# Performance work log

Measured on AMD Instinct MI355X. Metric: run time of the kernel, lower is better.

The kernel has to match this reference:

```python
import jax, jax.numpy as jnp
import numpy as np

B, N, K, C_IN, D = 4, 2048, 16, 480, 64
EPS = 1e-5


def _c1(x, w, b):
    # 1x1 Conv1d: x (B,C,N), w (O,C) -> (B,O,N)
    return jnp.einsum('oc,bcn->bon', w, x) + b[:, None]


def _c2(x, w, b):
    # 1x1 Conv2d: x (B,C,J,N), w (O,C) -> (B,O,J,N)
    return jnp.einsum('oc,bcjn->bojn', w, x) + b[:, None, None]


def _bn(x, g, b):
    # eval-mode BatchNorm2d with running_mean=0, running_var=1
    return x * (g / jnp.sqrt(1.0 + EPS))[:, None, None] + b[:, None, None]


def _mlp_res(x, w1, b1, w2, b2, ws, bs):
    return _c1(jax.nn.relu(_c1(x, w1, b1)), w2, b2) + _c1(x, ws, bs)


def _group(f, idx):
    # f (B,C,N), idx (B,K,N) int -> out[b,c,j,n] = f[b,c,idx[b,j,n]]  -> (B,C,K,N)
    return jax.vmap(lambda ff, ii: ff[:, ii])(f, idx)


def _knn_idx(xyz):
    # xyz (B,3,N) -> idx (B,K,N), excluding the self point (nearest neighbor)
    pts = xyz.transpose(0, 2, 1)  # (B,N,3)
    sq = jnp.sum(pts * pts, -1)
    d2 = sq[:, :, None] + sq[:, None, :] - 2.0 * jnp.einsum('bnd,bmd->bnm', pts, pts)
    _, idx = jax.lax.top_k(-d2, K + 1)  # (B,N,K+1), nearest first
    return idx.transpose(0, 2, 1)[:, 1:, :]  # drop self -> (B,K,N)


def _forward(idx, feature, xyz, bt1_w, bt1_b, bt2_w, bt2_b, bts_w, bts_b,
             q_w, q_b, k_w, k_b, v_w, v_b,
             fd1_w, fd1_b, fd_g, fd_bb, fd2_w, fd2_b,
             fg1_w, fg1_b, fg_g, fg_bb, fg2_w, fg2_b,
             at_w, at_b, m41_w, m41_b, m42_w, m42_b):
    x = _mlp_res(feature, bt1_w, bt1_b, bt2_w, bt2_b, bts_w, bts_b)  # (B,64,N)
    q = _c1(x, q_w, q_b)
    k = _c1(x, k_w, k_b)
    v = _c1(x, v_w, v_b)

    group_xyz = _group(xyz, idx)                       # (B,3,K,N)
    rel_xyz = xyz[:, :, None, :] - group_xyz           # (B,3,K,N)
    pos_enc = _c2(jax.nn.relu(_bn(_c2(rel_xyz, fd1_w, fd1_b), fd_g, fd_bb)), fd2_w, fd2_b)  # (B,64,K,N)

    k_local = _group(k, idx)                           # (B,64,K,N)
    v_local = _group(v, idx)
    qk_rel = q[:, :, None, :] - k_local
    attn = _c2(jax.nn.relu(_bn(_c2(qk_rel + pos_enc, fg1_w, fg1_b), fg_g, fg_bb)), fg2_w, fg2_b)  # (B,64,K,N)

    attn1 = attn.transpose(0, 1, 3, 2)                 # (B,64,N,K)
    # ConvTranspose2d(64,64,(4,1),(4,1)) with kernel==stride: out[b,o,4n+r,f] = sum_c x[b,c,n,f]*W[c,o,r] + bias[o]
    y = jnp.einsum('bcnf,cor->bonrf', attn1, at_w)
    y = y.reshape(y.shape[0], y.shape[1], -1, y.shape[4]) + at_b[None, :, None, None]  # (B,64,4N,K)
    attn = jax.nn.softmax(y, axis=1)

    value_rel = (v_local + pos_enc).transpose(0, 1, 3, 2)   # (B,64,N,K)
    value = jnp.repeat(value_rel, 4, axis=2)                # nearest upsample (4,1) -> (B,64,4N,K)

    res = jnp.einsum('bmnf,bmnf->bmn', attn, value)         # (B,64,4N)
    identity = jnp.repeat(x, 4, axis=2)                     # nearest upsample x4 -> (B,64,4N)
    res = res + identity
    completion = _c1(jax.nn.relu(_c1(res, m41_w, m41_b)), m42_w, m42_b)  # (B,3,4N)
    return completion, res


def setup_inputs() -> dict:
    key = jax.random.key(0)
    ks = jax.random.split(key, 24)
    i = iter(range(24))

    def w(shape):
        return (jax.random.normal(ks[next(i)], shape, dtype=jnp.float32) * 0.05)

    z = lambda n: jnp.zeros((n,), jnp.float32)
    o = lambda n: jnp.ones((n,), jnp.float32)
    return {
        'feature': jax.random.normal(ks[next(i)], (B, C_IN, N), dtype=jnp.float32),
        'xyz': jax.random.normal(ks[next(i)], (B, 3, N), dtype=jnp.float32),
        'bt1_w': w((D, C_IN)), 'bt1_b': z(D),
        'bt2_w': w((D, D)), 'bt2_b': z(D),
        'bts_w': w((D, C_IN)), 'bts_b': z(D),
        'q_w': w((D, D)), 'q_b': z(D),
        'k_w': w((D, D)), 'k_b': z(D),
        'v_w': w((D, D)), 'v_b': z(D),
        'fd1_w': w((D, 3)), 'fd1_b': z(D), 'fd_g': o(D), 'fd_bb': z(D),
        'fd2_w': w((D, D)), 'fd2_b': z(D),
        'fg1_w': w((4 * D, D)), 'fg1_b': z(4 * D), 'fg_g': o(4 * D), 'fg_bb': z(4 * D),
        'fg2_w': w((D, 4 * D)), 'fg2_b': z(D),
        'at_w': w((D, D, 4)), 'at_b': z(D),
        'm41_w': w((D, D)), 'm41_b': z(D),
        'm42_w': w((3, D)), 'm42_b': z(3),
    }


def reference(feature, xyz, bt1_w, bt1_b, bt2_w, bt2_b, bts_w, bts_b,
              q_w, q_b, k_w, k_b, v_w, v_b,
              fd1_w, fd1_b, fd_g, fd_bb, fd2_w, fd2_b,
              fg1_w, fg1_b, fg_g, fg_bb, fg2_w, fg2_b,
              at_w, at_b, m41_w, m41_b, m42_w, m42_b):
    idx = _knn_idx(xyz)
    return _forward(idx, feature, xyz, bt1_w, bt1_b, bt2_w, bt2_b, bts_w, bts_b,
                    q_w, q_b, k_w, k_b, v_w, v_b,
                    fd1_w, fd1_b, fd_g, fd_bb, fd2_w, fd2_b,
                    fg1_w, fg1_b, fg_g, fg_bb, fg2_w, fg2_b,
                    at_w, at_b, m41_w, m41_b, m42_w, m42_b)
```

## Files before the change

kernel.cpp:

```cpp
#include <hip/hip_runtime.h>

#define B_ 4
#define N_ 2048
#define K_ 16
#define CIN_ 480
#define UPN_ 8192
#define M_ (B_*N_*K_)
#define MX_ (B_*N_)
#define KCAP 448

#define KNN_BLK 2048
#define TR_BLK  1920
#define PREP_BLK 1047

typedef unsigned int u32;
typedef unsigned short u16;
typedef unsigned long long u64;
typedef __attribute__((ext_vector_type(8))) short short8;
typedef __attribute__((ext_vector_type(4))) float f32x4;

#define DEV static __device__ __forceinline__

DEV float b2f(u16 h){ return __uint_as_float(((u32)h)<<16); }
DEV u16 f2b(float f){
  u32 u = __float_as_uint(f);
  u32 r = u + 0x7fffu + ((u>>16)&1u);
  return (u16)(r>>16);
}
DEV u32 cvtpk(float a, float b){
  u32 r; asm("v_cvt_pk_bf16_f32 %0, %1, %2" : "=v"(r) : "v"(a), "v"(b));
  return r;
}
DEV u64 cvtpk4(float a, float b, float c, float d){
  return (u64)cvtpk(a,b) | ((u64)cvtpk(c,d)<<32);
}
DEV bool detect_bf(const void* fg){ return ((((const u32*)fg)[0]) & 0xFFFFu) == 0x3F80u; }
DEV float ld(const void* p, int i, bool bf){
  return bf ? b2f(((const u16*)p)[i]) : ((const float*)p)[i];
}
DEV u64 makekey(float d2, int m){
  u32 bits = __float_as_uint(d2);
  bits = (bits & 0x80000000u) ? ~bits : (bits | 0x80000000u);
  return ((u64)bits<<32) | (u32)m;
}
DEV int swz64 (int row, int colByte){ return row*128 + (colByte ^ ((row&7)<<4)); }
DEV int swz128(int row, int colByte){ return row*256 + (colByte ^ ((row&7)<<4)); }

__global__ __launch_bounds__(256) void setup_kernel(
    const void* __restrict__ feature, const void* __restrict__ xyz,
    const void* __restrict__ bt1_w, const void* __restrict__ bt1_b,
    const void* __restrict__ bt2_w, const void* __restrict__ bt2_b,
    const void* __restrict__ bts_w, const void* __restrict__ bts_b,
    const void* __restrict__ q_w, const void* __restrict__ q_b,
    const void* __restrict__ k_w, const void* __restrict__ k_b,
    const void* __restrict__ v_w, const void* __restrict__ v_b,
    const void* __restrict__ fd1_w, const void* __restrict__ fd1_b,
    const void* __restrict__ fd_g, const void* __restrict__ fd_bb,
    const void* __restrict__ fd2_w, const void* __restrict__ fd2_b,
    const void* __restrict__ fg1_w, const void* __restrict__ fg1_b,
    const void* __restrict__ fg_g, const void* __restrict__ fg_bb,
    const void* __restrict__ fg2_w, const void* __restrict__ fg2_b,
    const void* __restrict__ at_w, const void* __restrict__ at_b,
    const void* __restrict__ m41_w, const void* __restrict__ m41_b,
    const void* __restrict__ m42_w, const void* __restrict__ m42_b,
    float* __restrict__ W, u16* __restrict__ WB,
    u16* __restrict__ fxbT, float* __restrict__ fxyz, int* __restrict__ idx)
{
  __shared__ alignas(16) unsigned char smem[50208];
  int blkid = blockIdx.x;
  bool bf = detect_bf(fd_g);

  if(blkid < KNN_BLK){
    float* px = (float*)smem;
    float* py = px + N_;
    float* pz = py + N_;
    float* sq = pz + N_;
    u64*  sbuf = (u64*)(sq + N_);
    u64*  smin = sbuf + 4*KCAP;
    int*  scnt = (int*)(smin + 256);
    u64*  stau = (u64*)(scnt + 256);
    int bx = blkid & 511;
    int b = blkid >> 9;
    int base = b*3*N_;
    bool w0 = (bx==0);
    for(int i=threadIdx.x;i<N_;i+=256){
      float xx=ld(xyz,base+i,bf), yy=ld(xyz,base+N_+i,bf), zz=ld(xyz,base+2*N_+i,bf);
      px[i]=xx; py[i]=yy; pz[i]=zz; sq[i]=xx*xx+yy*yy+zz*zz;
      if(w0){ fxyz[base+i]=xx; fxyz[base+N_+i]=yy; fxyz[base+2*N_+i]=zz; }
    }
    __syncthreads();
    int w = threadIdx.x>>6, l = threadIdx.x&63;
    int q = bx*4 + w;
    float qx=px[q], qy=py[q], qz=pz[q], qs=sq[q];
    float d2c[32];
    u64 best=~0ull;
    #pragma unroll
    for(int j=0;j<32;j++){
      int m = l*32 + ((j+l)&31);
      float d2 = (qs+sq[m]) - 2.0f*(qx*px[m]+qy*py[m]+qz*pz[m]);
      d2c[j]=d2;
      u64 key = makekey(d2, m);
      best = key<best ? key : best;
    }
    smin[w*64+l]=best;
    __syncthreads();
    {
      int rank=0;
      for(int i=0;i<64;i++) rank += (smin[w*64+i] < best);
      if(rank==16) stau[w] = best;
    }
    __syncthreads();
    u64 tau = stau[w];
    int myc=0;
    #pragma unroll
    for(int j=0;j<32;j++){
      int m = l*32 + ((j+l)&31);
      myc += (makekey(d2c[j], m) <= tau);
    }
    scnt[w*64+l]=myc;
    __syncthreads();
    int off=0, tot=0;
    for(int i=0;i<64;i++){
      int c = scnt[w*64+i];
      tot += c;
      off += (i<l) ? c : 0;
    }
    #pragma unroll
    for(int j=0;j<32;j++){
      int m = l*32 + ((j+l)&31);
      u64 key = makekey(d2c[j], m);
      if(key<=tau && off<KCAP){ sbuf[w*KCAP+off]=key; off++; }
    }
    __syncthreads();
    if(tot>KCAP) tot=KCAP;
    for(int p=l; p<tot; p+=64){
      u64 kk = sbuf[w*KCAP+p];
      int rk=0;
      for(int i=0;i<tot;i++) rk += (sbuf[w*KCAP+i] < kk);
      if(rk>=1 && rk<17) idx[(b*K_+(rk-1))*N_+q] = ((int)(kk & 0xffffffffu)) & (N_-1);
    }
    return;
  }

  if(blkid < KNN_BLK + TR_BLK){
    u16 (*s)[34] = (u16(*)[34])smem;
    int t = blkid - KNN_BLK;
    int ntile = t & 31;  int rest = t >> 5;
    int ctile = rest % 15; int b = rest / 15;
    int tx = threadIdx.x & 31, ty = threadIdx.x >> 5;
    u64 base = (u64)b*CIN_*N_;
    #pragma unroll
    for(int r=0;r<4;r++){
      int c = ctile*32 + ty + r*8;
      u64 i = base + (u64)c*N_ + ntile*64 + tx*2;
      u32 v;
      if(bf) v = *(const u32*)((const u16*)feature + i);
      else {
        float a0=((const float*)feature)[i], a1=((const float*)feature)[i+1];
        v = (u32)f2b(a0) | ((u32)f2b(a1)<<16);
      }
      s[tx*2  ][ty + r*8] = (u16)v;
      s[tx*2+1][ty + r*8] = (u16)(v>>16);
    }
    __syncthreads();
    #pragma unroll
    for(int r=0;r<4;r++){
      int i2 = r*256 + threadIdx.x;
      int nrow = i2 >> 4, cp = i2 & 15;
      u32 v = *(const u32*)&s[nrow][cp*2];
      int n = ntile*64 + nrow;
      *(u32*)(fxbT + (u64)b*N_*CIN_ + (u64)n*CIN_ + ctile*32 + cp*2) = v;
    }
    return;
  }

  int t = (blkid - (KNN_BLK + TR_BLK))*256 + threadIdx.x;
  const float inv = 0.9999950000374997f;
  if(t < 30720) return; t -= 30720;
  if(t < 30720) return; t -= 30720;
  if(t < 4096) return; t -= 4096;
  if(t < 4096) return; t -= 4096;
  if(t < 4096) return; t -= 4096;
  if(t < 4096) return; t -= 4096;
  if(t < 256){
    int o=t>>2, j=t&3; float s = ld(fd_g,o,bf)*inv;
    W[77824+t] = (j<3) ? s*ld(fd1_w,o*3+j,bf) : (s*ld(fd1_b,o,bf) + ld(fd_bb,o,bf));
    return;
  } t -= 256;
  if(t < 4096) return; t -= 4096;
  if(t < 16384) return; t -= 16384;
  if(t < 256){ float s=ld(fg_g,t,bf)*inv; W[98560+t] = s*ld(fg1_b,t,bf) + ld(fg_bb,t,bf); return; } t -= 256;
  if(t < 16384) return; t -= 16384;
  if(t < 16384) return; t -= 16384;
  if(t < 4096){ int m=t>>6, o=t&63; W[131584+t] = ld(m41_w,o*64+m,bf); return; } t -= 4096;
  if(t < 192){ W[135680+t] = ld(m42_w,t,bf); return; } t -= 192;
  if(t < 64){ W[135872+t] = ld(bt1_b,t,bf); return; } t -= 64;
  if(t < 64){ W[135936+t] = ld(bts_b,t,bf); return; } t -= 64;
  if(t < 64){ W[136000+t] = ld(bt2_b,t,bf); return; } t -= 64;
  if(t < 64){ W[136064+t] = ld(q_b,t,bf); return; } t -= 64;
  if(t < 64){ W[136128+t] = ld(k_b,t,bf); return; } t -= 64;
  if(t < 64){ W[136192+t] = ld(v_b,t,bf); return; } t -= 64;
  if(t < 64){ W[136256+t] = ld(fd2_b,t,bf); return; } t -= 64;
  if(t < 64){ W[136320+t] = ld(fg2_b,t,bf); return; } t -= 64;
  if(t < 64){ W[136384+t] = ld(at_b,t,bf); return; } t -= 64;
  if(t < 64){ W[136448+t] = ld(m41_b,t,bf); return; } t -= 64;
  if(t < 3){ W[136512+t] = ld(m42_b,t,bf); return; } t -= 3;
  if(t < 16384){ int o=t>>6; float s=ld(fg_g,o,bf)*inv; WB[t] = f2b(s*ld(fg1_w,t,bf)); return; } t -= 16384;
  if(t < 16384){ WB[16384+t] = f2b(ld(fg2_w,t,bf)); return; } t -= 16384;
  if(t < 16384){ int j=t>>6, c=t&63;
                 WB[32768+t] = f2b(ld(at_w,(c*64+(j&63))*4+(j>>6),bf)); return; } t -= 16384;
  if(t < 256){ W[136576+t] = ld(at_b,t&63,bf); return; } t -= 256;
  if(t < 4096){ WB[49152+t] = f2b(ld(fd2_w,t,bf)); return; } t -= 4096;
  if(t < 30720){ WB[53248+t] = f2b(ld(bt1_w,t,bf)); return; } t -= 30720;
  if(t < 30720){ WB[83968+t] = f2b(ld(bts_w,t,bf)); return; } t -= 30720;
  if(t < 4096){ WB[114688+t] = f2b(ld(bt2_w,t,bf)); return; } t -= 4096;
  if(t < 4096){ WB[118784+t] = f2b(ld(q_w,t,bf)); return; } t -= 4096;
  if(t < 4096){ WB[122880+t] = f2b(ld(k_w,t,bf)); return; } t -= 4096;
  if(t < 4096){ WB[126976+t] = f2b(ld(v_w,t,bf)); return; }
}

__global__ __launch_bounds__(256) void gemm480_mfma(const u16* __restrict__ A,
    const u16* __restrict__ Wt, const float* __restrict__ bias,
    u16* __restrict__ hout, float* __restrict__ xsout)
{
  int tid=threadIdx.x, w=tid>>6, lane=tid&63;
  int rbase=(blockIdx.x*4+w)*16;
  int cbase=blockIdx.y*64;
  int lr=lane&15, lk=(lane>>4)*8;
  f32x4 acc[4];
  #pragma unroll
  for(int j=0;j<4;j++) acc[j]=(f32x4){0.f,0.f,0.f,0.f};
  for(int kc=0;kc<CIN_;kc+=32){
    short8 a = *(const short8*)(A + (u64)(rbase+lr)*CIN_ + kc + lk);
    #pragma unroll
    for(int tj=0;tj<4;tj++){
      short8 bb = *(const short8*)(Wt + (u64)(cbase+tj*16+lr)*CIN_ + kc + lk);
      acc[tj] = __builtin_amdgcn_mfma_f32_16x16x32_bf16(a, bb, acc[tj], 0,0,0);
    }
  }
  int rq=(lane>>4)*4;
  #pragma unroll
  for(int tj=0;tj<4;tj++){
    int col = cbase + tj*16 + lr;
    float bv = bias[col];
    #pragma unroll
    for(int reg=0;reg<4;reg++){
      u64 row = rbase + rq + reg;
      float vv = acc[tj][reg] + bv;
      if(blockIdx.y==0) hout[row*64 + col] = f2b(fmaxf(vv,0.f));
      else              xsout[row*64 + (col-64)] = vv;
    }
  }
}

__global__ __launch_bounds__(256) void x_mfma(const u16* __restrict__ A,
    const u16* __restrict__ Wt, const float* __restrict__ bias,
    const float* __restrict__ xs, float* __restrict__ x, u16* __restrict__ xb)
{
  int tid=threadIdx.x, w=tid>>6, lane=tid&63;
  int rbase=(blockIdx.x*4+w)*16;
  int lr=lane&15, lk=(lane>>4)*8;
  f32x4 acc[4];
  #pragma unroll
  for(int j=0;j<4;j++) acc[j]=(f32x4){0.f,0.f,0.f,0.f};
  #pragma unroll
  for(int kc=0;kc<64;kc+=32){
    short8 a = *(const short8*)(A + (u64)(rbase+lr)*64 + kc + lk);
    #pragma unroll
    for(int tj=0;tj<4;tj++){
      short8 bb = *(const short8*)(Wt + (u64)(tj*16+lr)*64 + kc + lk);
      acc[tj] = __builtin_amdgcn_mfma_f32_16x16x32_bf16(a, bb, acc[tj], 0,0,0);
    }
  }
  int rq=(lane>>4)*4;
  #pragma unroll
  for(int tj=0;tj<4;tj++){
    int col = tj*16 + lr;
    float bv = bias[col];
    #pragma unroll
    for(int reg=0;reg<4;reg++){
      u64 row = rbase + rq + reg;
      float vv = acc[tj][reg] + bv + xs[row*64+col];
      x[row*64+col] = vv;
      xb[row*64+col] = f2b(vv);
    }
  }
}

__global__ __launch_bounds__(256) void qkv_mfma(const u16* __restrict__ A,
    const u16* __restrict__ Wt, const float* __restrict__ bias, float* __restrict__ qkv)
{
  int tid=threadIdx.x, w=tid>>6, lane=tid&63;
  int rbase=(blockIdx.x*4+w)*16;
  int cbase=blockIdx.y*64;
  int lr=lane&15, lk=(lane>>4)*8;
  f32x4 acc[4];
  #pragma unroll
  for(int j=0;j<4;j++) acc[j]=(f32x4){0.f,0.f,0.f,0.f};
  #pragma unroll
  for(int kc=0;kc<64;kc+=32){
    short8 a = *(const short8*)(A + (u64)(rbase+lr)*64 + kc + lk);
    #pragma unroll
    for(int tj=0;tj<4;tj++){
      short8 bb = *(const short8*)(Wt + (u64)(cbase+tj*16+lr)*64 + kc + lk);
      acc[tj] = __builtin_amdgcn_mfma_f32_16x16x32_bf16(a, bb, acc[tj], 0,0,0);
    }
  }
  int rq=(lane>>4)*4;
  #pragma unroll
  for(int tj=0;tj<4;tj++){
    int col = cbase + tj*16 + lr;
    float bv = bias[col];
    #pragma unroll
    for(int reg=0;reg<4;reg++){
      u64 row = rbase + rq + reg;
      qkv[row*192 + col] = acc[tj][reg] + bv;
    }
  }
}

__global__ __launch_bounds__(256) void fused_chain(
    const int* __restrict__ idx, const float* __restrict__ fxyz,
    const float* __restrict__ qkv, const float* __restrict__ x,
    const float* __restrict__ fd1f,
    const u16* __restrict__ Wfd2, const float* __restrict__ bfd2,
    const u16* __restrict__ Wfg1, const float* __restrict__ bfg1,
    const u16* __restrict__ Wfg2, const float* __restrict__ bfg2,
    const u16* __restrict__ Wat,  const float* __restrict__ bat,
    const void* __restrict__ det, void* __restrict__ out)
{
  __shared__ alignas(16) unsigned char lds[32768];
  int tid = threadIdx.x;
  int w = tid>>6, lane = tid&63;
  int lr = lane&15, lk = (lane>>4)*8, rq = (lane>>4)*4;

  int erow = tid>>2, ecg = tid&3;
  int el = erow>>4, ef = erow&15;
  int bn_e = blockIdx.x*4 + el;
  int b_e = bn_e>>11, n_e = bn_e&(N_-1);
  int jn = idx[(b_e*K_+ef)*N_ + n_e] & (N_-1);

  {
    const float* xb = fxyz + (u64)b_e*3*N_;
    float rx = xb[n_e]      - xb[jn];
    float ry = xb[N_+n_e]   - xb[N_+jn];
    float rz = xb[2*N_+n_e] - xb[2*N_+jn];
    #pragma unroll
    for(int gg=0; gg<4; gg++){
      float tv[4];
      #pragma unroll
      for(int j=0;j<4;j++){
        f32x4 wv = *(const f32x4*)(fd1f + ((ecg*4+gg)*4+j)*4);
        tv[j] = fmaxf(wv[0]*rx + wv[1]*ry + wv[2]*rz + wv[3], 0.f);
      }
      *(u64*)(lds + swz64(erow, (ecg*4+gg)*8)) = cvtpk4(tv[0],tv[1],tv[2],tv[3]);
    }
  }
  __syncthreads();

  {
    f32x4 acc[4];
    #pragma unroll
    for(int i=0;i<4;i++) acc[i]=(f32x4){0.f,0.f,0.f,0.f};
    #pragma unroll
    for(int kc=0;kc<64;kc+=32){
      short8 wf = *(const short8*)(Wfd2 + (u64)(w*16+lr)*64 + kc + lk);
      #pragma unroll
      for(int ti=0;ti<4;ti++){
        short8 tf = *(const short8*)(lds + swz64(ti*16+lr, (kc+lk)*2));
        acc[ti] = __builtin_amdgcn_mfma_f32_16x16x32_bf16(wf, tf, acc[ti], 0,0,0);
      }
    }
    f32x4 b4 = *(const f32x4*)(bfd2 + w*16 + rq);
    #pragma unroll
    for(int ti=0;ti<4;ti++)
      *(u64*)(lds + 8192 + swz64(ti*16+lr, (w*16+rq)*2)) =
        cvtpk4(acc[ti][0]+b4[0], acc[ti][1]+b4[1], acc[ti][2]+b4[2], acc[ti][3]+b4[3]);
  }
  __syncthreads();

  {
    int mg = ecg*16;
    const float* qrow = qkv + (u64)(b_e*N_+n_e)*192 + mg;
    const float* krow = qkv + (u64)(b_e*N_+jn)*192 + 64 + mg;
    const float* vrow = qkv + (u64)(b_e*N_+jn)*192 + 128 + mg;
    #pragma unroll
    for(int g2=0; g2<4; g2++){
      f32x4 qv = *(const f32x4*)(qrow + g2*4);
      f32x4 kv = *(const f32x4*)(krow + g2*4);
      f32x4 vv = *(const f32x4*)(vrow + g2*4);
      int cb = (mg + g2*4)*2;
      u64 pw = *(const u64*)(lds + 8192 + swz64(erow, cb));
      float p0=b2f((u16)pw), p1=b2f((u16)(pw>>16)), p2=b2f((u16)(pw>>32)), p3=b2f((u16)(pw>>48));
      *(u64*)(lds + swz64(erow, cb)) =
        cvtpk4(qv[0]-kv[0]+p0, qv[1]-kv[1]+p1, qv[2]-kv[2]+p2, qv[3]-kv[3]+p3);
      *(u64*)(lds + 8192 + swz64(erow, cb)) =
        cvtpk4(vv[0]+p0, vv[1]+p1, vv[2]+p2, vv[3]+p3);
    }
  }
  __syncthreads();

  float vreg[16];
  #pragma unroll
  for(int f2=0; f2<16; f2++)
    vreg[f2] = b2f(*(const u16*)(lds + 8192 + swz64(w*16+f2, lane*2)));

  f32x4 gacc[4];
  #pragma unroll
  for(int i=0;i<4;i++) gacc[i]=(f32x4){0.f,0.f,0.f,0.f};
  #pragma unroll
  for(int half=0; half<2; half++){
    {
      f32x4 hacc[2][4];
      #pragma unroll
      for(int i=0;i<2;i++)
        #pragma unroll
        for(int j=0;j<4;j++) hacc[i][j]=(f32x4){0.f,0.f,0.f,0.f};
      #pragma unroll
      for(int kc=0;kc<64;kc+=32){
        short8 wf[2], af[4];
        #pragma unroll
        for(int ti=0;ti<2;ti++)
          wf[ti] = *(const short8*)(Wfg1 + (u64)(half*128 + w*32 + ti*16 + lr)*64 + kc + lk);
        #pragma unroll
        for(int tj=0;tj<4;tj++)
          af[tj] = *(const short8*)(lds + swz64(tj*16+lr, (kc+lk)*2));
        #pragma unroll
        for(int ti=0;ti<2;ti++)
          #pragma unroll
          for(int tj=0;tj<4;tj++)
            hacc[ti][tj] = __builtin_amdgcn_mfma_f32_16x16x32_bf16(wf[ti], af[tj], hacc[ti][tj], 0,0,0);
      }
      #pragma unroll
      for(int ti=0;ti<2;ti++){
        f32x4 b4 = *(const f32x4*)(bfg1 + half*128 + w*32 + ti*16 + rq);
        #pragma unroll
        for(int tj=0;tj<4;tj++){
          int row = tj*16 + lr;
          *(u64*)(lds + 16384 + swz128(row, (w*32+ti*16+rq)*2)) =
            cvtpk4(fmaxf(hacc[ti][tj][0]+b4[0],0.f), fmaxf(hacc[ti][tj][1]+b4[1],0.f),
                   fmaxf(hacc[ti][tj][2]+b4[2],0.f), fmaxf(hacc[ti][tj][3]+b4[3],0.f));
        }
      }
    }
    __syncthreads();
    #pragma unroll
    for(int kc=0;kc<128;kc+=32){
      short8 wf = *(const short8*)(Wfg2 + (u64)(w*16+lr)*256 + half*128 + kc + lk);
      #pragma unroll
      for(int tj=0;tj<4;tj++){
        short8 hf = *(const short8*)(lds + 16384 + swz128(tj*16+lr, (kc+lk)*2));
        gacc[tj] = __builtin_amdgcn_mfma_f32_16x16x32_bf16(wf, hf, gacc[tj], 0,0,0);
      }
    }
    __syncthreads();
  }

  {
    f32x4 b4 = *(const f32x4*)(bfg2 + w*16 + rq);
    #pragma unroll
    for(int tj=0;tj<4;tj++)
      *(u64*)(lds + swz64(tj*16+lr, (w*16+rq)*2)) =
        cvtpk4(gacc[tj][0]+b4[0], gacc[tj][1]+b4[1], gacc[tj][2]+b4[2], gacc[tj][3]+b4[3]);
  }
  __syncthreads();

  float aout[4];
  int srow = tid>>2, sub = tid&3;
  #pragma unroll
  for(int r=0;r<4;r++){
    {
      f32x4 acc[4];
      #pragma unroll
      for(int i=0;i<4;i++) acc[i]=(f32x4){0.f,0.f,0.f,0.f};
      #pragma unroll
      for(int kc=0;kc<64;kc+=32){
        short8 wf = *(const short8*)(Wat + (u64)(r*64 + w*16 + lr)*64 + kc + lk);
        #pragma unroll
        for(int tj=0;tj<4;tj++){
          short8 gf = *(const short8*)(lds + swz64(tj*16+lr, (kc+lk)*2));
          acc[tj] = __builtin_amdgcn_mfma_f32_16x16x32_bf16(wf, gf, acc[tj], 0,0,0);
        }
      }
      f32x4 b4 = *(const f32x4*)(bat + r*64 + w*16 + rq);
      #pragma unroll
      for(int tj=0;tj<4;tj++)
        *(u64*)(lds + 16384 + swz64(tj*16+lr, (w*16+rq)*2)) =
          cvtpk4(acc[tj][0]+b4[0], acc[tj][1]+b4[1], acc[tj][2]+b4[2], acc[tj][3]+b4[3]);
    }
    __syncthreads();
    {
      float yv[16];
      uint4 pk0 = *(const uint4*)(lds + 16384 + swz64(srow, sub*32));
      uint4 pk1 = *(const uint4*)(lds + 16384 + swz64(srow, sub*32 + 16));
      yv[0]=__uint_as_float(pk0.x<<16); yv[1]=__uint_as_float(pk0.x&0xffff0000u);
      yv[2]=__uint_as_float(pk0.y<<16); yv[3]=__uint_as_float(pk0.y&0xffff0000u);
      yv[4]=__uint_as_float(pk0.z<<16); yv[5]=__uint_as_float(pk0.z&0xffff0000u);
      yv[6]=__uint_as_float(pk0.w<<16); yv[7]=__uint_as_float(pk0.w&0xffff0000u);
      yv[8]=__uint_as_float(pk1.x<<16); yv[9]=__uint_as_float(pk1.x&0xffff0000u);
      yv[10]=__uint_as_float(pk1.y<<16); yv[11]=__uint_as_float(pk1.y&0xffff0000u);
      yv[12]=__uint_as_float(pk1.z<<16); yv[13]=__uint_as_float(pk1.z&0xffff0000u);
      yv[14]=__uint_as_float(pk1.w<<16); yv[15]=__uint_as_float(pk1.w&0xffff0000u);
      float mx = yv[0];
      #pragma unroll
      for(int m=1;m<16;m++) mx = fmaxf(mx, yv[m]);
      mx = fmaxf(mx, __shfl_xor(mx, 1));
      mx = fmaxf(mx, __shfl_xor(mx, 2));
      float sm = 0.f;
      #pragma unroll
      for(int m=0;m<16;m++){ float e = __expf(yv[m]-mx); yv[m]=e; sm+=e; }
      sm += __shfl_xor(sm, 1);
      sm += __shfl_xor(sm, 2);
      float rinv = 1.0f/sm;
      uint4 o0, o1;
      o0.x = cvtpk(yv[0]*rinv, yv[1]*rinv);  o0.y = cvtpk(yv[2]*rinv, yv[3]*rinv);
      o0.z = cvtpk(yv[4]*rinv, yv[5]*rinv);  o0.w = cvtpk(yv[6]*rinv, yv[7]*rinv);
      o1.x = cvtpk(yv[8]*rinv, yv[9]*rinv);  o1.y = cvtpk(yv[10]*rinv, yv[11]*rinv);
      o1.z = cvtpk(yv[12]*rinv, yv[13]*rinv); o1.w = cvtpk(yv[14]*rinv, yv[15]*rinv);
      *(uint4*)(lds + 8192 + swz64(srow, sub*32))      = o0;
      *(uint4*)(lds + 8192 + swz64(srow, sub*32 + 16)) = o1;
    }
    __syncthreads();
    {
      float a = 0.f;
      #pragma unroll
      for(int f2=0; f2<16; f2++)
        a += b2f(*(const u16*)(lds + 8192 + swz64(w*16+f2, lane*2))) * vreg[f2];
      aout[r] = a;
    }
  }

  int bn = blockIdx.x*4 + w;
  int b = bn>>11, n = bn&(N_-1);
  float xv = x[(u64)bn*64 + lane];
  u64 off = 98304 + ((u64)(b*64+lane))*UPN_ + (u64)n*4;
  if(detect_bf(det)){
    *(u64*)((u16*)out + off) = cvtpk4(aout[0]+xv, aout[1]+xv, aout[2]+xv, aout[3]+xv);
  } else {
    f32x4 pk = {aout[0]+xv, aout[1]+xv, aout[2]+xv, aout[3]+xv};
    *(f32x4*)((float*)out + off) = pk;
  }
}

__global__ __launch_bounds__(128) void comp_kernel(
  const float* __restrict__ m41T, const float* __restrict__ m41b,
  const float* __restrict__ m42f, const float* __restrict__ m42b,
  const void* __restrict__ det, void* __restrict__ out)
{
  int tid = threadIdx.x;
  int wv = tid>>6, lane = tid&63;
  int half = lane>>5, l32 = lane&31;
  int g = blockIdx.x*64 + wv*32 + l32;
  int un = g & (UPN_-1);
  int b = g >> 13;
  bool bf = detect_bf(det);
  float acc[32];
  #pragma unroll
  for(int o=0;o<32;o++) acc[o] = m41b[half*32+o];
  if(bf){
    const u16* rr = (const u16*)out + 98304 + (u64)b*64*UPN_ + un;
    for(int c=0;c<64;c++){
      float rv = b2f(rr[(u64)c*UPN_]);
      const float* w = m41T + c*64 + half*32;
      #pragma unroll
      for(int o=0;o<32;o++) acc[o] += w[o]*rv;
    }
  } else {
    const float* rr = (const float*)out + 98304 + (u64)b*64*UPN_ + un;
    for(int c=0;c<64;c++){
      float rv = rr[(u64)c*UPN_];
      const float* w = m41T + c*64 + half*32;
      #pragma unroll
      for(int o=0;o<32;o++) acc[o] += w[o]*rv;
    }
  }
  float c0=0.f, c1=0.f, c2=0.f;
  #pragma unroll
  for(int o=0;o<32;o++){
    float hv = fmaxf(acc[o],0.f);
    c0 += m42f[half*32+o]*hv; c1 += m42f[64+half*32+o]*hv; c2 += m42f[128+half*32+o]*hv;
  }
  c0 += __shfl_xor(c0, 32);
  c1 += __shfl_xor(c1, 32);
  c2 += __shfl_xor(c2, 32);
  if(half==0){
    c0 += m42b[0]; c1 += m42b[1]; c2 += m42b[2];
    u64 base = (u64)b*3*UPN_ + un;
    if(bf){
      u16* cp = (u16*)out;
      cp[base]=f2b(c0); cp[base+UPN_]=f2b(c1); cp[base+2*UPN_]=f2b(c2);
    } else {
      float* cp = (float*)out;
      cp[base]=c0; cp[base+UPN_]=c1; cp[base+2*UPN_]=c2;
    }
  }
}

extern "C" void kernel_launch(void* const* d_in, const int* in_sizes, int n_in,
                              void* d_out, int out_size, void* d_ws, size_t ws_size,
                              hipStream_t stream)
{
  (void)in_sizes; (void)n_in; (void)out_size; (void)ws_size;
  const void* feature=d_in[0];
  const void* xyz   =d_in[1];
  const void* bt1_w =d_in[2];  const void* bt1_b=d_in[3];
  const void* bt2_w =d_in[4];  const void* bt2_b=d_in[5];
  const void* bts_w =d_in[6];  const void* bts_b=d_in[7];
  const void* q_w   =d_in[8];  const void* q_b =d_in[9];
  const void* k_w   =d_in[10]; const void* k_b =d_in[11];
  const void* v_w   =d_in[12]; const void* v_b =d_in[13];
  const void* fd1_w =d_in[14]; const void* fd1_b=d_in[15];
  const void* fd_g  =d_in[16]; const void* fd_bb=d_in[17];
  const void* fd2_w =d_in[18]; const void* fd2_b=d_in[19];
  const void* fg1_w =d_in[20]; const void* fg1_b=d_in[21];
  const void* fg_g  =d_in[22]; const void* fg_bb=d_in[23];
  const void* fg2_w =d_in[24]; const void* fg2_b=d_in[25];
  const void* at_w  =d_in[26]; const void* at_b =d_in[27];
  const void* m41_w =d_in[28]; const void* m41_b=d_in[29];
  const void* m42_w =d_in[30]; const void* m42_b=d_in[31];

  char* ws=(char*)d_ws;
  float* W   =(float*)(ws);
  u16*  WB   =(u16*)  (ws + 589824);
  int*  idx  =(int*)  (ws + 851968);
  float* x   =(float*)(ws + 1376256);
  float* qkv =(float*)(ws + 3473408);
  u16*  h    =(u16*)  (ws + 9764864);
  float* xs  =(float*)(ws + 10813440);
  u16*  xb   =(u16*)  (ws + 12910592);
  u16*  fxbT =(u16*)  (ws + 114622464);
  float* fxyz=(float*)(ws + 122486784);

  const float* W_fd1f = W+77824;
  const float* W_fg1fb= W+98560;
  const float* W_m41T = W+131584;
  const float* W_m42  = W+135680;
  const float* Wb_g480= W+135872;
  const float* Wb_bt2 = W+136000;
  const float* Wb_qkv = W+136064;
  const float* Wb_fd2 = W+136256;
  const float* Wb_fg2 = W+136320;
  const float* Wb_m41 = W+136448;
  const float* Wb_m42 = W+136512;
  const float* W_atb256 = W+136576;
  const u16* WB_fg1  = WB;
  const u16* WB_fg2  = WB+16384;
  const u16* WB_at   = WB+32768;
  const u16* WB_fd2  = WB+49152;
  const u16* WB_g480 = WB+53248;
  const u16* WB_bt2  = WB+114688;
  const u16* WB_qkv  = WB+118784;

  setup_kernel<<<KNN_BLK+TR_BLK+PREP_BLK,256,0,stream>>>(feature, xyz,
      bt1_w,bt1_b,bt2_w,bt2_b,bts_w,bts_b,q_w,q_b,k_w,k_b,
      v_w,v_b,fd1_w,fd1_b,fd_g,fd_bb,fd2_w,fd2_b,fg1_w,fg1_b,fg_g,fg_bb,fg2_w,fg2_b,
      at_w,at_b,m41_w,m41_b,m42_w,m42_b,W,WB,fxbT,fxyz,idx);
  gemm480_mfma<<<dim3(MX_/64,2),256,0,stream>>>(fxbT, WB_g480, Wb_g480, h, xs);
  x_mfma<<<MX_/64,256,0,stream>>>(h, WB_bt2, Wb_bt2, xs, x, xb);
  qkv_mfma<<<dim3(MX_/64,3),256,0,stream>>>(xb, WB_qkv, Wb_qkv, qkv);
  fused_chain<<<B_*N_/4,256,0,stream>>>(idx, fxyz, qkv, x, W_fd1f,
      WB_fd2, Wb_fd2, WB_fg1, W_fg1fb, WB_fg2, Wb_fg2, WB_at, W_atb256, fd_g, d_out);
  comp_kernel<<<512,128,0,stream>>>(W_m41T, Wb_m41, W_m42, Wb_m42, fd_g, d_out);
}
```

Measured before the change: 262.1 us.

## Fuse x and qkv GEMMs, fold final MLP into fused chain epilogue

Merges the x projection and the qkv projection into one kernel that keeps the bf16 x tile in LDS instead of writing and rereading an xb buffer. It also removes comp_kernel by computing the m41/m42 pointwise MLP in the fused_chain epilogue, reusing the freshly computed output values from registers/LDS instead of rereading them from global memory. This cuts two launches and some global traffic, but adds serial per-wave work (a 64-iteration loop plus a 12-lane reduction) to the tail of fused_chain, which may lengthen that kernel. The operand order of the MFMA is swapped so outputs land transposed, allowing vector stores.

```diff
diff --git a/kernel.cpp b/kernel.cpp
--- a/kernel.cpp
+++ b/kernel.cpp
@@ -253,68 +253,64 @@
   }
 }
 
-__global__ __launch_bounds__(256) void x_mfma(const u16* __restrict__ A,
-    const u16* __restrict__ Wt, const float* __restrict__ bias,
-    const float* __restrict__ xs, float* __restrict__ x, u16* __restrict__ xb)
+__global__ __launch_bounds__(256) void xqkv_mfma(const u16* __restrict__ A,
+    const u16* __restrict__ Wbt2, const float* __restrict__ bbt2,
+    const float* __restrict__ xs,
+    const u16* __restrict__ Wqkv, const float* __restrict__ bqkv,
+    float* __restrict__ x, float* __restrict__ qkvout)
 {
+  __shared__ alignas(16) unsigned char lds[8192];
   int tid=threadIdx.x, w=tid>>6, lane=tid&63;
-  int rbase=(blockIdx.x*4+w)*16;
-  int lr=lane&15, lk=(lane>>4)*8;
-  f32x4 acc[4];
+  int lr=lane&15, lk=(lane>>4)*8, rq=(lane>>4)*4;
+  unsigned char* Lw = lds + w*2048;
+  u64 rbase=(u64)(blockIdx.x*4+w)*16;
+
+  {
+    f32x4 ax[4];
+    #pragma unroll
+    for(int i=0;i<4;i++) ax[i]=(f32x4){0.f,0.f,0.f,0.f};
+    #pragma unroll
+    for(int kc=0;kc<64;kc+=32){
+      short8 hf = *(const short8*)(A + (rbase+lr)*64 + kc + lk);
+      #pragma unroll
+      for(int t=0;t<4;t++){
+        short8 wf = *(const short8*)(Wbt2 + (u64)(t*16+lr)*64 + kc + lk);
+        ax[t] = __builtin_amdgcn_mfma_f32_16x16x32_bf16(wf, hf, ax[t], 0,0,0);
+      }
+    }
+    #pragma unroll
+    for(int t=0;t<4;t++){
+      f32x4 bb = *(const f32x4*)(bbt2 + t*16 + rq);
+      f32x4 sv = *(const f32x4*)(xs + (rbase+lr)*64 + t*16 + rq);
+      f32x4 xv;
+      #pragma unroll
+      for(int reg=0;reg<4;reg++) xv[reg] = ax[t][reg] + bb[reg] + sv[reg];
+      *(f32x4*)(x + (rbase+lr)*64 + t*16 + rq) = xv;
+      *(u64*)(Lw + swz64(lr, (t*16+rq)*2)) = cvtpk4(xv[0],xv[1],xv[2],xv[3]);
+    }
+  }
+  __syncthreads();
   #pragma unroll
-  for(int j=0;j<4;j++) acc[j]=(f32x4){0.f,0.f,0.f,0.f};
-  #pragma unroll
-  for(int kc=0;kc<64;kc+=32){
-    short8 a = *(const short8*)(A + (u64)(rbase+lr)*64 + kc + lk);
-    #pragma unroll
-    for(int tj=0;tj<4;tj++){
-      short8 bb = *(const short8*)(Wt + (u64)(tj*16+lr)*64 + kc + lk);
-      acc[tj] = __builtin_amdgcn_mfma_f32_16x16x32_bf16(a, bb, acc[tj], 0,0,0);
-    }
-  }
-  int rq=(lane>>4)*4;
-  #pragma unroll
-  for(int tj=0;tj<4;tj++){
-    int col = tj*16 + lr;
-    float bv = bias[col];
-    #pragma unroll
-    for(int reg=0;reg<4;reg++){
-      u64 row = rbase + rq + reg;
-      float vv = acc[tj][reg] + bv + xs[row*64+col];
-      x[row*64+col] = vv;
-      xb[row*64+col] = f2b(vv);
-    }
-  }
-}
-
-__global__ __launch_bounds__(256) void qkv_mfma(const u16* __restrict__ A,
-    const u16* __restrict__ Wt, const float* __restrict__ bias, float* __restrict__ qkv)
-{
-  int tid=threadIdx.x, w=tid>>6, lane=tid&63;
-  int rbase=(blockIdx.x*4+w)*16;
-  int cbase=blockIdx.y*64;
-  int lr=lane&15, lk=(lane>>4)*8;
-  f32x4 acc[4];
-  #pragma unroll
-  for(int j=0;j<4;j++) acc[j]=(f32x4){0.f,0.f,0.f,0.f};
-  #pragma unroll
-  for(int kc=0;kc<64;kc+=32){
-    short8 a = *(const short8*)(A + (u64)(rbase+lr)*64 + kc + lk);
-    #pragma unroll
-    for(int tj=0;tj<4;tj++){
-      short8 bb = *(const short8*)(Wt + (u64)(cbase+tj*16+lr)*64 + kc + lk);
-      acc[tj] = __builtin_amdgcn_mfma_f32_16x16x32_bf16(a, bb, acc[tj], 0,0,0);
-    }
-  }
-  int rq=(lane>>4)*4;
-  #pragma unroll
-  for(int tj=0;tj<4;tj++){
-    int col = cbase + tj*16 + lr;
-    float bv = bias[col];
-    #pragma unroll
-    for(int reg=0;reg<4;reg++){
-      u64 row = rbase + rq + reg;
-      qkv[row*192 + col] = acc[tj][reg] + bv;
+  for(int g=0;g<3;g++){
+    f32x4 aq[4];
+    #pragma unroll
+    for(int i=0;i<4;i++) aq[i]=(f32x4){0.f,0.f,0.f,0.f};
+    #pragma unroll
+    for(int kc=0;kc<64;kc+=32){
+      short8 hf = *(const short8*)(Lw + swz64(lr, (kc+lk)*2));
+      #pragma unroll
+      for(int t=0;t<4;t++){
+        short8 wf = *(const short8*)(Wqkv + (u64)(g*64+t*16+lr)*64 + kc + lk);
+        aq[t] = __builtin_amdgcn_mfma_f32_16x16x32_bf16(wf, hf, aq[t], 0,0,0);
+      }
+    }
+    #pragma unroll
+    for(int t=0;t<4;t++){
+      f32x4 bq = *(const f32x4*)(bqkv + g*64 + t*16 + rq);
+      f32x4 ov;
+      #pragma unroll
+      for(int reg=0;reg<4;reg++) ov[reg] = aq[t][reg] + bq[reg];
+      *(f32x4*)(qkvout + (rbase+lr)*192 + g*64 + t*16 + rq) = ov;
     }
   }
 }
@@ -327,6 +323,8 @@
     const u16* __restrict__ Wfg1, const float* __restrict__ bfg1,
     const u16* __restrict__ Wfg2, const float* __restrict__ bfg2,
     const u16* __restrict__ Wat,  const float* __restrict__ bat,
+    const float* __restrict__ cm41T, const float* __restrict__ cm41b,
+    const float* __restrict__ cm42f, const float* __restrict__ cm42b,
     const void* __restrict__ det, void* __restrict__ out)
 {
   __shared__ alignas(16) unsigned char lds[32768];
@@ -534,65 +532,42 @@
   int b = bn>>11, n = bn&(N_-1);
   float xv = x[(u64)bn*64 + lane];
   u64 off = 98304 + ((u64)(b*64+lane))*UPN_ + (u64)n*4;
-  if(detect_bf(det)){
-    *(u64*)((u16*)out + off) = cvtpk4(aout[0]+xv, aout[1]+xv, aout[2]+xv, aout[3]+xv);
+  bool bf = detect_bf(det);
+  float rv0, rv1, rv2, rv3;
+  if(bf){
+    u64 pk = cvtpk4(aout[0]+xv, aout[1]+xv, aout[2]+xv, aout[3]+xv);
+    *(u64*)((u16*)out + off) = pk;
+    rv0 = b2f((u16)pk); rv1 = b2f((u16)(pk>>16));
+    rv2 = b2f((u16)(pk>>32)); rv3 = b2f((u16)(pk>>48));
   } else {
     f32x4 pk = {aout[0]+xv, aout[1]+xv, aout[2]+xv, aout[3]+xv};
     *(f32x4*)((float*)out + off) = pk;
-  }
-}
-
-__global__ __launch_bounds__(128) void comp_kernel(
-  const float* __restrict__ m41T, const float* __restrict__ m41b,
-  const float* __restrict__ m42f, const float* __restrict__ m42b,
-  const void* __restrict__ det, void* __restrict__ out)
-{
-  int tid = threadIdx.x;
-  int wv = tid>>6, lane = tid&63;
-  int half = lane>>5, l32 = lane&31;
-  int g = blockIdx.x*64 + wv*32 + l32;
-  int un = g & (UPN_-1);
-  int b = g >> 13;
-  bool bf = detect_bf(det);
-  float acc[32];
-  #pragma unroll
-  for(int o=0;o<32;o++) acc[o] = m41b[half*32+o];
-  if(bf){
-    const u16* rr = (const u16*)out + 98304 + (u64)b*64*UPN_ + un;
+    rv0 = pk[0]; rv1 = pk[1]; rv2 = pk[2]; rv3 = pk[3];
+  }
+  float* L = (float*)(lds + w*1024);
+  *(f32x4*)(L + lane*4) = (f32x4){rv0, rv1, rv2, rv3};
+  f32x4 acc4;
+  {
+    float bo = cm41b[lane];
+    acc4 = (f32x4){bo, bo, bo, bo};
     for(int c=0;c<64;c++){
-      float rv = b2f(rr[(u64)c*UPN_]);
-      const float* w = m41T + c*64 + half*32;
-      #pragma unroll
-      for(int o=0;o<32;o++) acc[o] += w[o]*rv;
-    }
-  } else {
-    const float* rr = (const float*)out + 98304 + (u64)b*64*UPN_ + un;
-    for(int c=0;c<64;c++){
-      float rv = rr[(u64)c*UPN_];
-      const float* w = m41T + c*64 + half*32;
-      #pragma unroll
-      for(int o=0;o<32;o++) acc[o] += w[o]*rv;
-    }
-  }
-  float c0=0.f, c1=0.f, c2=0.f;
-  #pragma unroll
-  for(int o=0;o<32;o++){
-    float hv = fmaxf(acc[o],0.f);
-    c0 += m42f[half*32+o]*hv; c1 += m42f[64+half*32+o]*hv; c2 += m42f[128+half*32+o]*hv;
-  }
-  c0 += __shfl_xor(c0, 32);
-  c1 += __shfl_xor(c1, 32);
-  c2 += __shfl_xor(c2, 32);
-  if(half==0){
-    c0 += m42b[0]; c1 += m42b[1]; c2 += m42b[2];
-    u64 base = (u64)b*3*UPN_ + un;
-    if(bf){
-      u16* cp = (u16*)out;
-      cp[base]=f2b(c0); cp[base+UPN_]=f2b(c1); cp[base+2*UPN_]=f2b(c2);
-    } else {
-      float* cp = (float*)out;
-      cp[base]=c0; cp[base+UPN_]=c1; cp[base+2*UPN_]=c2;
-    }
+      float wv = cm41T[c*64 + lane];
+      f32x4 rr = *(const f32x4*)(L + c*4);
+      acc4[0] += wv*rr[0]; acc4[1] += wv*rr[1];
+      acc4[2] += wv*rr[2]; acc4[3] += wv*rr[3];
+    }
+  }
+  f32x4 h2 = {fmaxf(acc4[0],0.f), fmaxf(acc4[1],0.f),
+              fmaxf(acc4[2],0.f), fmaxf(acc4[3],0.f)};
+  *(f32x4*)(L + lane*4) = h2;
+  if(lane < 12){
+    int coord = lane>>2, r2 = lane&3;
+    float sum = cm42b[coord];
+    for(int o=0;o<64;o++)
+      sum += cm42f[coord*64+o] * L[o*4 + r2];
+    u64 base = (u64)b*3*UPN_ + (u64)coord*UPN_ + (u64)n*4 + r2;
+    if(bf) ((u16*)out)[base] = f2b(sum);
+    else   ((float*)out)[base] = sum;
   }
 }
 
@@ -627,7 +602,6 @@
   float* qkv =(float*)(ws + 3473408);
   u16*  h    =(u16*)  (ws + 9764864);
   float* xs  =(float*)(ws + 10813440);
-  u16*  xb   =(u16*)  (ws + 12910592);
   u16*  fxbT =(u16*)  (ws + 114622464);
   float* fxyz=(float*)(ws + 122486784);
 
@@ -656,9 +630,8 @@
       v_w,v_b,fd1_w,fd1_b,fd_g,fd_bb,fd2_w,fd2_b,fg1_w,fg1_b,fg_g,fg_bb,fg2_w,fg2_b,
       at_w,at_b,m41_w,m41_b,m42_w,m42_b,W,WB,fxbT,fxyz,idx);
   gemm480_mfma<<<dim3(MX_/64,2),256,0,stream>>>(fxbT, WB_g480, Wb_g480, h, xs);
-  x_mfma<<<MX_/64,256,0,stream>>>(h, WB_bt2, Wb_bt2, xs, x, xb);
-  qkv_mfma<<<dim3(MX_/64,3),256,0,stream>>>(xb, WB_qkv, Wb_qkv, qkv);
+  xqkv_mfma<<<MX_/64,256,0,stream>>>(h, WB_bt2, Wb_bt2, xs, WB_qkv, Wb_qkv, x, qkv);
   fused_chain<<<B_*N_/4,256,0,stream>>>(idx, fxyz, qkv, x, W_fd1f,
-      WB_fd2, Wb_fd2, WB_fg1, W_fg1fb, WB_fg2, Wb_fg2, WB_at, W_atb256, fd_g, d_out);
-  comp_kernel<<<512,128,0,stream>>>(W_m41T, Wb_m41, W_m42, Wb_m42, fd_g, d_out);
-}
+      WB_fd2, Wb_fd2, WB_fg1, W_fg1fb, WB_fg2, Wb_fg2, WB_at, W_atb256,
+      W_m41T, Wb_m41, W_m42, Wb_m42, fd_g, d_out);
+}
```

After: 252.2 us. 3.8% less time.
